# Optimization experiments

Hardware: AMD Instinct MI355X
Metric: run time of the kernel (lower is better)

## Reference

```python
import jax, jax.numpy as jnp
import numpy as np

L, B, H, E, V = 64, 2048, 1024, 50, 256  # seq_len, batch, hidden, char_emb, char_vocab
PAD = 0


def setup_inputs() -> dict:
    key = jax.random.key(0)
    ks = jax.random.split(key, 10)
    s = 1.0 / np.sqrt(H)  # torch LSTM default init scale
    emb = jax.random.normal(ks[0], (V, E), jnp.float32)
    emb = emb.at[PAD].set(0.0)  # padding_idx row
    return {
        "input": jax.random.randint(ks[1], (L, B), 0, V, jnp.int32),
        "h0": jax.random.normal(ks[2], (1, B, H), jnp.float32),
        "c0": jax.random.normal(ks[3], (1, B, H), jnp.float32),
        "emb": emb,
        "W_ih": jax.random.uniform(ks[4], (4 * H, E), jnp.float32, -s, s),
        "W_hh": jax.random.uniform(ks[5], (4 * H, H), jnp.float32, -s, s),
        "b_ih": jax.random.uniform(ks[6], (4 * H,), jnp.float32, -s, s),
        "b_hh": jax.random.uniform(ks[7], (4 * H,), jnp.float32, -s, s),
        "W_proj": jax.random.uniform(ks[8], (V, H), jnp.float32, -s, s),
        "b_proj": jax.random.uniform(ks[9], (V,), jnp.float32, -s, s),
    }


def reference(input, h0, c0, emb, W_ih, W_hh, b_ih, b_hh, W_proj, b_proj):
    # char embedding lookup: (L, B, E)
    x = emb[input]
    b = b_ih + b_hh

    def step(carry, x_t):
        h, c = carry  # (B, H) each
        gates = x_t @ W_ih.T + h @ W_hh.T + b  # (B, 4H), torch gate order i,f,g,o
        i, f, g, o = jnp.split(gates, 4, axis=-1)
        c_new = jax.nn.sigmoid(f) * c + jax.nn.sigmoid(i) * jnp.tanh(g)
        h_new = jax.nn.sigmoid(o) * jnp.tanh(c_new)
        return (h_new, c_new), h_new

    (hT, cT), hs = jax.lax.scan(step, (h0[0], c0[0]), x)
    # per-step linear projection of hidden state (same math as looped Linear)
    scores = hs @ W_proj.T + b_proj  # (L, B, V)
    return scores, hT[None], cT[None]
```

## Files before the change

kernel.cpp:

```cpp
#include <hip/hip_runtime.h>
#include <hip/hip_bf16.h>
#include <cstdint>
#include <cstddef>

#define LSEQ  64
#define BATCH 2048
#define HID   1024
#define NGATE 4096
#define VOC   256
#define EMBD  50

using bf16 = __hip_bfloat16;
typedef __attribute__((ext_vector_type(8))) __bf16 bf16x8;
typedef __attribute__((ext_vector_type(4))) float  f32x4;

__device__ __forceinline__ void gload_lds16(const void* g, void* l) {
  __builtin_amdgcn_global_load_lds(
      (const __attribute__((address_space(1))) unsigned int*)g,
      (__attribute__((address_space(3))) unsigned int*)l, 16, 0, 0);
}

__device__ __forceinline__ float sigf(float x) {
  x = fminf(fmaxf(x, -30.f), 30.f);
  return 1.f / (1.f + __expf(-x));
}
__device__ __forceinline__ float tanh_f(float x) {
  x = fminf(fmaxf(x, -15.f), 15.f);
  float e = __expf(2.f * x);
  return (e - 1.f) / (e + 1.f);
}

__device__ __forceinline__ void store_h_sys(bf16* p, float v) {
  union { __hip_bfloat16 b; unsigned short u; } cv;
  cv.b = __float2bfloat16(v);
  unsigned int d = cv.u;
  asm volatile("global_store_short %0, %1, off sc0 sc1" :: "v"(p), "v"(d) : "memory");
}


__global__ void k_prep_whh(const float* __restrict__ W, bf16* __restrict__ Wr) {
  size_t i = (size_t)blockIdx.x * 256 + threadIdx.x;
  int k  = (int)(i & 1023);
  int np = (int)(i >> 10);
  int T = np >> 7, w = np & 127;
  int wc = w >> 6, g = (w >> 4) & 3, hl = w & 15;
  int grow = g * HID + T * 32 + wc * 16 + hl;
  Wr[i] = __float2bfloat16(W[(size_t)grow * HID + k]);
}

__global__ void k_prep_embw(const float* __restrict__ emb, const float* __restrict__ W_ih,
                            const float* __restrict__ b_ih, const float* __restrict__ b_hh,
                            float* __restrict__ embW) {
  size_t i = (size_t)blockIdx.x * 256 + threadIdx.x;
  int np = (int)(i & 4095);
  int v  = (int)(i >> 12);
  int T = np >> 7, w = np & 127;
  int wc = w >> 6, g = (w >> 4) & 3, hl = w & 15;
  int grow = g * HID + T * 32 + wc * 16 + hl;
  float s = b_ih[grow] + b_hh[grow];
  #pragma unroll 10
  for (int e = 0; e < EMBD; ++e)
    s += emb[(size_t)v * EMBD + e] * W_ih[(size_t)grow * EMBD + e];
  embW[i] = s;
}

__global__ void k_prep_wp(const float* __restrict__ Wp_f, bf16* __restrict__ Wp) {
  size_t i = (size_t)blockIdx.x * 256 + threadIdx.x;
  Wp[i] = __float2bfloat16(Wp_f[i]);
}

__global__ void k_init_state(const float* __restrict__ h0, bf16* __restrict__ hs,
                             int* __restrict__ arr) {
  size_t i = (size_t)blockIdx.x * 256 + threadIdx.x;
  hs[i] = __float2bfloat16(h0[i]);
  if (i < 8320) arr[i] = 0;
}

__global__ __launch_bounds__(512) void g_persist(
    const float* __restrict__ c0, const bf16* __restrict__ Wr,
    bf16* __restrict__ hs, int* __restrict__ arr,
    const float* __restrict__ embW, const int* __restrict__ input,
    float* __restrict__ out, int nslots)
{
  __shared__ __align__(16) bf16 lsA[3 * 256 * 64];
  __shared__ __align__(16) bf16 lsB[3 * 128 * 64];

  const int tid  = threadIdx.x;
  const int wave = tid >> 6, lane = tid & 63;
  const int wr = wave >> 1, wc = wave & 1;
  const int hl = lane & 15, q = lane >> 4;

  const int u  = blockIdx.x >> 3;
  const int by = (blockIdx.x & 7) | ((u & 3) << 3);
  const int bx = u >> 2;
  const int bxbase = bx * 256;

  const bf16* Bsrc = Wr + (size_t)by * 128 * HID;

  size_t offA0, offA1, offA2, offA3;
  {
    int g0 = tid,      r0 = g0 >> 3, c0v = (g0 & 7) ^ (r0 & 7);
    int g1 = 512+tid,  r1 = g1 >> 3, c1v = (g1 & 7) ^ (r1 & 7);
    int g2 = 1024+tid, r2 = g2 >> 3, c2v = (g2 & 7) ^ (r2 & 7);
    int g3 = 1536+tid, r3 = g3 >> 3, c3v = (g3 & 7) ^ (r3 & 7);
    offA0 = (size_t)r0 * HID + c0v * 8;
    offA1 = (size_t)r1 * HID + c1v * 8;
    offA2 = (size_t)r2 * HID + c2v * 8;
    offA3 = (size_t)r3 * HID + c3v * 8;
  }
  bf16* dA = lsA + wave * 512;
  bf16* dB = lsB + wave * 512;

  int aofs0[4], aofs1[4], bofs0[4], bofs1[4];
  #pragma unroll
  for (int m = 0; m < 4; ++m) {
    int row = wr * 64 + m * 16 + hl;
    aofs0[m] = row * 64 + ((q ^ (hl & 7)) * 8);
    aofs1[m] = row * 64 + (((4 + q) ^ (hl & 7)) * 8);
  }
  #pragma unroll
  for (int n = 0; n < 4; ++n) {
    int row = wc * 64 + n * 16 + hl;
    bofs0[n] = row * 64 + ((q ^ (hl & 7)) * 8);
    bofs1[n] = row * 64 + (((4 + q) ^ (hl & 7)) * 8);
  }

  const int h_idx = by * 32 + wc * 16 + hl;
  float creg[4][4];
  #pragma unroll
  for (int m = 0; m < 4; ++m)
    #pragma unroll
    for (int r = 0; r < 4; ++r)
      creg[m][r] = c0[(size_t)(bxbase + wr * 64 + m * 16 + q * 4 + r) * HID + h_idx];

  const float* ewc = embW + (size_t)(by * 128 + wc * 64);
  const size_t slotE = (size_t)BATCH * HID;

#define SSTG0(S_) { gload_lds16(pA0, dA + (S_)*16384);         pA0 += 64;  \
                    gload_lds16(pA1, dA + (S_)*16384 + 4096);  pA1 += 64;  \
                    gload_lds16(pA2, dA + (S_)*16384 + 8192);  pA2 += 64; }
#define SSTG1(S_) { gload_lds16(pA3, dA + (S_)*16384 + 12288); pA3 += 64;  \
                    gload_lds16(pB0, dB + (S_)*8192);          pB0 += 64;  \
                    gload_lds16(pB1, dB + (S_)*8192 + 4096);   pB1 += 64; }

#define SPHASE(Ab_, Bb_, AO_, BO_, STG_) {                                  \
    bf16x8 aF[4], bF[4];                                                    \
    _Pragma("unroll")                                                       \
    for (int m = 0; m < 4; ++m) aF[m] = *(const bf16x8*)((Ab_) + AO_[m]);   \
    _Pragma("unroll")                                                       \
    for (int n = 0; n < 4; ++n) bF[n] = *(const bf16x8*)((Bb_) + BO_[n]);   \
    STG_;                                                                   \
    __builtin_amdgcn_s_barrier();                                           \
    asm volatile("s_waitcnt lgkmcnt(0)" ::: "memory");                      \
    __builtin_amdgcn_sched_barrier(0);                                      \
    __builtin_amdgcn_s_setprio(1);                                          \
    _Pragma("unroll")                                                       \
    for (int m = 0; m < 4; ++m)                                             \
      _Pragma("unroll")                                                     \
      for (int n = 0; n < 4; ++n)                                           \
        acc[m][n] = __builtin_amdgcn_mfma_f32_16x16x32_bf16(aF[m], bF[n], acc[m][n], 0, 0, 0); \
    __builtin_amdgcn_s_setprio(0);                                          \
  }

  for (int t = 0; t < LSEQ; ++t) {
    if (t) {
      if (tid == 0) {
        int it = 0;
        while (__hip_atomic_load(&arr[(t * 8 + bx) * 16], __ATOMIC_RELAXED,
                                 __HIP_MEMORY_SCOPE_AGENT) < 32 && ++it < (1 << 20))
          __builtin_amdgcn_s_sleep(2);
      }
      __syncthreads();
      __builtin_amdgcn_sched_barrier(0);
    }

    const bf16* Asrc = hs + (size_t)(t % nslots) * slotE + (size_t)bxbase * HID;
    const bf16 *pA0 = Asrc + offA0, *pA1 = Asrc + offA1;
    const bf16 *pA2 = Asrc + offA2, *pA3 = Asrc + offA3;
    const bf16 *pB0 = Bsrc + offA0, *pB1 = Bsrc + offA1;

    f32x4 acc[4][4] = {};

    SSTG0(0); SSTG1(0);
    SSTG0(1); SSTG1(1);
    __builtin_amdgcn_sched_barrier(0);

    int cur = 0, st = 2;
    for (int T = 0; T < 15; ++T) {
      asm volatile("s_waitcnt vmcnt(6)" ::: "memory");
      __builtin_amdgcn_s_barrier();
      const bf16* Ab = lsA + cur * 16384;
      const bf16* Bb = lsB + cur * 8192;
      if (T < 14) {
        SPHASE(Ab, Bb, aofs0, bofs0, SSTG0(st));
        SPHASE(Ab, Bb, aofs1, bofs1, SSTG1(st));
      } else {
        SPHASE(Ab, Bb, aofs0, bofs0, );
        SPHASE(Ab, Bb, aofs1, bofs1, );
      }
      cur = (cur == 2) ? 0 : cur + 1;
      st  = (st  == 2) ? 0 : st  + 1;
    }
    asm volatile("s_waitcnt vmcnt(0)" ::: "memory");
    __builtin_amdgcn_s_barrier();
    {
      const bf16* Ab = lsA + cur * 16384;
      const bf16* Bb = lsB + cur * 8192;
      SPHASE(Ab, Bb, aofs0, bofs0, );
      SPHASE(Ab, Bb, aofs1, bofs1, );
    }
    __builtin_amdgcn_sched_barrier(0);

    bf16* hout = hs + (size_t)((t + 1) % nslots) * slotE;
    #pragma unroll
    for (int m = 0; m < 4; ++m) {
      const int b0 = bxbase + wr * 64 + m * 16 + q * 4;
      const int4 iv = *(const int4*)(input + (size_t)t * BATCH + b0);
      #pragma unroll
      for (int r = 0; r < 4; ++r) {
        const int idx = (&iv.x)[r];
        const float* ew = ewc + (size_t)idx * NGATE;
        float gi = acc[m][0][r] + ew[hl];
        float gf = acc[m][1][r] + ew[16 + hl];
        float gg = acc[m][2][r] + ew[32 + hl];
        float go = acc[m][3][r] + ew[48 + hl];
        float cn = sigf(gf) * creg[m][r] + sigf(gi) * tanh_f(gg);
        float hn = sigf(go) * tanh_f(cn);
        creg[m][r] = cn;
        const size_t off = (size_t)(b0 + r) * HID + h_idx;
        store_h_sys(hout + off, hn);
        if (t == LSEQ - 1) {
          out[(size_t)LSEQ * BATCH * VOC + off] = hn;
          out[(size_t)LSEQ * BATCH * VOC + slotE + off] = cn;
        }
      }
    }

    __syncthreads();
    if (tid == 0)
      __hip_atomic_fetch_add(&arr[((t + 1) * 8 + bx) * 16], 1, __ATOMIC_RELAXED,
                             __HIP_MEMORY_SCOPE_AGENT);
  }
#undef SSTG0
#undef SSTG1
#undef SPHASE
}

template<int MODE>
__global__ __launch_bounds__(512) void g8(
    const bf16* __restrict__ Abase, const bf16* __restrict__ Bbase,
    const float* __restrict__ b_proj, float* __restrict__ out,
    int kc, int nslots)
{
  __shared__ __align__(16) bf16 lsA[3 * 256 * 64];
  __shared__ __align__(16) bf16 lsB[3 * 128 * 64];

  const int tid  = threadIdx.x;
  const int wave = tid >> 6, lane = tid & 63;
  const int wr = wave >> 1, wc = wave & 1;
  const int hl = lane & 15, q = lane >> 4;

  const int bx = blockIdx.x, by = blockIdx.y;

  int t_local = bx >> 3;
  int slot = (kc + 1 + t_local) % nslots;
  const bf16* Asrc = Abase + ((size_t)slot * BATCH + (size_t)(bx & 7) * 256) * HID;
  const bf16* Bsrc = Bbase + (size_t)by * 128 * HID;

  const bf16 *pA0, *pA1, *pA2, *pA3, *pB0, *pB1;
  {
    int g0 = tid,      r0 = g0 >> 3, c0v = (g0 & 7) ^ (r0 & 7);
    int g1 = 512+tid,  r1 = g1 >> 3, c1v = (g1 & 7) ^ (r1 & 7);
    int g2 = 1024+tid, r2 = g2 >> 3, c2v = (g2 & 7) ^ (r2 & 7);
    int g3 = 1536+tid, r3 = g3 >> 3, c3v = (g3 & 7) ^ (r3 & 7);
    pA0 = Asrc + (size_t)r0 * HID + c0v * 8;
    pA1 = Asrc + (size_t)r1 * HID + c1v * 8;
    pA2 = Asrc + (size_t)r2 * HID + c2v * 8;
    pA3 = Asrc + (size_t)r3 * HID + c3v * 8;
    pB0 = Bsrc + (size_t)r0 * HID + c0v * 8;
    pB1 = Bsrc + (size_t)r1 * HID + c1v * 8;
  }
  bf16* dA = lsA + wave * 512;
  bf16* dB = lsB + wave * 512;

  int aofs0[4], aofs1[4], bofs0[4], bofs1[4];
  #pragma unroll
  for (int m = 0; m < 4; ++m) {
    int row = wr * 64 + m * 16 + hl;
    aofs0[m] = row * 64 + ((q ^ (hl & 7)) * 8);
    aofs1[m] = row * 64 + (((4 + q) ^ (hl & 7)) * 8);
  }
  #pragma unroll
  for (int n = 0; n < 4; ++n) {
    int row = wc * 64 + n * 16 + hl;
    bofs0[n] = row * 64 + ((q ^ (hl & 7)) * 8);
    bofs1[n] = row * 64 + (((4 + q) ^ (hl & 7)) * 8);
  }

  f32x4 acc[4][4] = {};

#define STG_P0(S_) { gload_lds16(pA0, dA + (S_)*16384);         pA0 += 64;  \
                     gload_lds16(pA1, dA + (S_)*16384 + 4096);  pA1 += 64;  \
                     gload_lds16(pA2, dA + (S_)*16384 + 8192);  pA2 += 64; }
#define STG_P1(S_) { gload_lds16(pA3, dA + (S_)*16384 + 12288); pA3 += 64;  \
                     gload_lds16(pB0, dB + (S_)*8192);          pB0 += 64;  \
                     gload_lds16(pB1, dB + (S_)*8192 + 4096);   pB1 += 64; }

#define PHASE(Ab_, Bb_, AO_, BO_, STG_) {                                   \
    bf16x8 aF[4], bF[4];                                                    \
    _Pragma("unroll")                                                       \
    for (int m = 0; m < 4; ++m) aF[m] = *(const bf16x8*)((Ab_) + AO_[m]);   \
    _Pragma("unroll")                                                       \
    for (int n = 0; n < 4; ++n) bF[n] = *(const bf16x8*)((Bb_) + BO_[n]);   \
    STG_;                                                                   \
    __builtin_amdgcn_s_barrier();                                           \
    asm volatile("s_waitcnt lgkmcnt(0)" ::: "memory");                      \
    __builtin_amdgcn_sched_barrier(0);                                      \
    __builtin_amdgcn_s_setprio(1);                                          \
    _Pragma("unroll")                                                       \
    for (int m = 0; m < 4; ++m)                                             \
      _Pragma("unroll")                                                     \
      for (int n = 0; n < 4; ++n)                                           \
        acc[m][n] = __builtin_amdgcn_mfma_f32_16x16x32_bf16(aF[m], bF[n], acc[m][n], 0, 0, 0); \
    __builtin_amdgcn_s_setprio(0);                                          \
  }

  STG_P0(0); STG_P1(0);
  STG_P0(1); STG_P1(1);
  __builtin_amdgcn_sched_barrier(0);

  int cur = 0, st = 2;
  for (int T = 0; T < 15; ++T) {
    asm volatile("s_waitcnt vmcnt(6)" ::: "memory");
    __builtin_amdgcn_s_barrier();
    const bf16* Ab = lsA + cur * 16384;
    const bf16* Bb = lsB + cur * 8192;
    if (T < 14) {
      PHASE(Ab, Bb, aofs0, bofs0, STG_P0(st));
      PHASE(Ab, Bb, aofs1, bofs1, STG_P1(st));
    } else {
      PHASE(Ab, Bb, aofs0, bofs0, );
      PHASE(Ab, Bb, aofs1, bofs1, );
    }
    cur = (cur == 2) ? 0 : cur + 1;
    st  = (st  == 2) ? 0 : st  + 1;
  }
  asm volatile("s_waitcnt vmcnt(0)" ::: "memory");
  __builtin_amdgcn_s_barrier();
  {
    const bf16* Ab = lsA + cur * 16384;
    const bf16* Bb = lsB + cur * 8192;
    PHASE(Ab, Bb, aofs0, bofs0, );
    PHASE(Ab, Bb, aofs1, bofs1, );
  }

#undef STG_P0
#undef STG_P1
#undef PHASE

  const int qrow = q * 4;
  const int t_glob = kc + (bx >> 3);
  float* os = out + (size_t)t_glob * BATCH * VOC;
  const int b0base = (bx & 7) * 256 + wr * 64;
  #pragma unroll
  for (int m = 0; m < 4; ++m) {
    #pragma unroll
    for (int n = 0; n < 4; ++n) {
      const int v = by * 128 + wc * 64 + n * 16 + hl;
      const float bp = b_proj[v];
      #pragma unroll
      for (int r = 0; r < 4; ++r)
        os[(size_t)(b0base + m * 16 + qrow + r) * VOC + v] = acc[m][n][r] + bp;
    }
  }
}


extern "C" void kernel_launch(void* const* d_in, const int* in_sizes, int n_in,
                              void* d_out, int out_size, void* d_ws, size_t ws_size,
                              hipStream_t stream)
{
  (void)in_sizes; (void)n_in; (void)out_size; (void)ws_size;
  const int*   input  = (const int*)  d_in[0];
  const float* h0     = (const float*)d_in[1];
  const float* c0     = (const float*)d_in[2];
  const float* emb    = (const float*)d_in[3];
  const float* W_ih   = (const float*)d_in[4];
  const float* W_hh   = (const float*)d_in[5];
  const float* b_ih   = (const float*)d_in[6];
  const float* b_hh   = (const float*)d_in[7];
  const float* W_proj = (const float*)d_in[8];
  const float* b_proj = (const float*)d_in[9];
  float* out = (float*)d_out;

  char* ws = (char*)d_ws;
  bf16*  Wr   = (bf16*)(ws);
  bf16*  Wp   = (bf16*)(ws + 8388608);
  float* embW = (float*)(ws + 8912896);
  int*   arr  = (int*)  (ws + 13107200);
  bf16*  hs   = (bf16*) (ws + 13140480);
  const int nslots = 65;

  k_prep_whh <<<16384, 256, 0, stream>>>(W_hh, Wr);
  k_prep_wp  <<<1024,  256, 0, stream>>>(W_proj, Wp);
  k_prep_embw<<<4096,  256, 0, stream>>>(emb, W_ih, b_ih, b_hh, embW);
  k_init_state<<<8192, 256, 0, stream>>>(h0, hs, arr);

  g_persist<<<dim3(256), 512, 0, stream>>>(c0, Wr, hs, arr, embW, input, out, nslots);

  g8<1><<<dim3(8 * 64, 2), 512, 0, stream>>>(hs, Wp, b_proj, out, 0, nslots);
}
```

Measured before the change: 2.166 ms.

## Split persistent LSTM tiles to 128x128 with 4-stage K=32 pipeline

The persistent recurrent kernel moves from 256 blocks of 512 threads with 256x128 output tiles to 512 blocks of 256 threads with 128x128 tiles, two blocks per CU. The K loop now uses 32-wide tiles in a 4-deep LDS ring instead of 64-wide tiles in a 3-deep ring. The embedding-gate table is relaid so each (token, hidden) entry holds the four gates as one float4 load. Per-step barriers are indexed over 16 batch groups, and a vmcnt wait is added before signalling so h stores land first. The aim is better latency hiding and overlap between blocks per CU, at the cost of reading the W_hh tile twice as often.

```diff
diff --git a/kernel.cpp b/kernel.cpp
--- a/kernel.cpp
+++ b/kernel.cpp
@@ -52,11 +52,10 @@
                             const float* __restrict__ b_ih, const float* __restrict__ b_hh,
                             float* __restrict__ embW) {
   size_t i = (size_t)blockIdx.x * 256 + threadIdx.x;
-  int np = (int)(i & 4095);
-  int v  = (int)(i >> 12);
-  int T = np >> 7, w = np & 127;
-  int wc = w >> 6, g = (w >> 4) & 3, hl = w & 15;
-  int grow = g * HID + T * 32 + wc * 16 + hl;
+  int v     = (int)(i >> 12);
+  int h_col = (int)((i >> 2) & 1023);
+  int g     = (int)(i & 3);
+  int grow = g * HID + h_col;
   float s = b_ih[grow] + b_hh[grow];
   #pragma unroll 10
   for (int e = 0; e < EMBD; ++e)
@@ -73,57 +72,41 @@
                              int* __restrict__ arr) {
   size_t i = (size_t)blockIdx.x * 256 + threadIdx.x;
   hs[i] = __float2bfloat16(h0[i]);
-  if (i < 8320) arr[i] = 0;
-}
-
-__global__ __launch_bounds__(512) void g_persist(
+  if (i < 16640) arr[i] = 0;
+}
+
+__global__ __launch_bounds__(256, 2) void g_persist(
     const float* __restrict__ c0, const bf16* __restrict__ Wr,
     bf16* __restrict__ hs, int* __restrict__ arr,
     const float* __restrict__ embW, const int* __restrict__ input,
     float* __restrict__ out, int nslots)
 {
-  __shared__ __align__(16) bf16 lsA[3 * 256 * 64];
-  __shared__ __align__(16) bf16 lsB[3 * 128 * 64];
+  __shared__ __align__(16) bf16 lsA[4 * 128 * 32];
+  __shared__ __align__(16) bf16 lsB[4 * 128 * 32];
 
   const int tid  = threadIdx.x;
   const int wave = tid >> 6, lane = tid & 63;
   const int wr = wave >> 1, wc = wave & 1;
   const int hl = lane & 15, q = lane >> 4;
 
-  const int u  = blockIdx.x >> 3;
-  const int by = (blockIdx.x & 7) | ((u & 3) << 3);
+  const int u  = (int)blockIdx.x >> 3;
+  const int by = ((int)blockIdx.x & 7) | ((u & 3) << 3);
   const int bx = u >> 2;
-  const int bxbase = bx * 256;
+  const int bxbase = bx * 128;
 
   const bf16* Bsrc = Wr + (size_t)by * 128 * HID;
 
-  size_t offA0, offA1, offA2, offA3;
-  {
-    int g0 = tid,      r0 = g0 >> 3, c0v = (g0 & 7) ^ (r0 & 7);
-    int g1 = 512+tid,  r1 = g1 >> 3, c1v = (g1 & 7) ^ (r1 & 7);
-    int g2 = 1024+tid, r2 = g2 >> 3, c2v = (g2 & 7) ^ (r2 & 7);
-    int g3 = 1536+tid, r3 = g3 >> 3, c3v = (g3 & 7) ^ (r3 & 7);
-    offA0 = (size_t)r0 * HID + c0v * 8;
-    offA1 = (size_t)r1 * HID + c1v * 8;
-    offA2 = (size_t)r2 * HID + c2v * 8;
-    offA3 = (size_t)r3 * HID + c3v * 8;
-  }
+  const size_t off0 = (size_t)(tid >> 2) * HID +
+                      ((((tid & 3) ^ ((tid >> 4) & 3)) << 3));
   bf16* dA = lsA + wave * 512;
   bf16* dB = lsB + wave * 512;
 
-  int aofs0[4], aofs1[4], bofs0[4], bofs1[4];
-  #pragma unroll
-  for (int m = 0; m < 4; ++m) {
-    int row = wr * 64 + m * 16 + hl;
-    aofs0[m] = row * 64 + ((q ^ (hl & 7)) * 8);
-    aofs1[m] = row * 64 + (((4 + q) ^ (hl & 7)) * 8);
-  }
-  #pragma unroll
-  for (int n = 0; n < 4; ++n) {
-    int row = wc * 64 + n * 16 + hl;
-    bofs0[n] = row * 64 + ((q ^ (hl & 7)) * 8);
-    bofs1[n] = row * 64 + (((4 + q) ^ (hl & 7)) * 8);
-  }
+  const int kk = ((q ^ ((hl >> 2) & 3)) << 3);
+  int aofs[4], bofs[4];
+  #pragma unroll
+  for (int m = 0; m < 4; ++m) aofs[m] = (wr * 64 + m * 16 + hl) * 32 + kk;
+  #pragma unroll
+  for (int n = 0; n < 4; ++n) bofs[n] = (wc * 64 + n * 16 + hl) * 32 + kk;
 
   const int h_idx = by * 32 + wc * 16 + hl;
   float creg[4][4];
@@ -133,24 +116,21 @@
     for (int r = 0; r < 4; ++r)
       creg[m][r] = c0[(size_t)(bxbase + wr * 64 + m * 16 + q * 4 + r) * HID + h_idx];
 
-  const float* ewc = embW + (size_t)(by * 128 + wc * 64);
   const size_t slotE = (size_t)BATCH * HID;
 
-#define SSTG0(S_) { gload_lds16(pA0, dA + (S_)*16384);         pA0 += 64;  \
-                    gload_lds16(pA1, dA + (S_)*16384 + 4096);  pA1 += 64;  \
-                    gload_lds16(pA2, dA + (S_)*16384 + 8192);  pA2 += 64; }
-#define SSTG1(S_) { gload_lds16(pA3, dA + (S_)*16384 + 12288); pA3 += 64;  \
-                    gload_lds16(pB0, dB + (S_)*8192);          pB0 += 64;  \
-                    gload_lds16(pB1, dB + (S_)*8192 + 4096);   pB1 += 64; }
-
-#define SPHASE(Ab_, Bb_, AO_, BO_, STG_) {                                  \
+#define KSTG(S_) { gload_lds16(pA0, dA + (S_)*4096);        pA0 += 32;  \
+                   gload_lds16(pA1, dA + (S_)*4096 + 2048); pA1 += 32;  \
+                   gload_lds16(pB0, dB + (S_)*4096);        pB0 += 32;  \
+                   gload_lds16(pB1, dB + (S_)*4096 + 2048); pB1 += 32; }
+
+#define KTILE(CUR_) {                                                       \
+    const bf16* Ab = lsA + (CUR_) * 4096;                                   \
+    const bf16* Bb = lsB + (CUR_) * 4096;                                   \
     bf16x8 aF[4], bF[4];                                                    \
     _Pragma("unroll")                                                       \
-    for (int m = 0; m < 4; ++m) aF[m] = *(const bf16x8*)((Ab_) + AO_[m]);   \
-    _Pragma("unroll")                                                       \
-    for (int n = 0; n < 4; ++n) bF[n] = *(const bf16x8*)((Bb_) + BO_[n]);   \
-    STG_;                                                                   \
-    __builtin_amdgcn_s_barrier();                                           \
+    for (int m = 0; m < 4; ++m) aF[m] = *(const bf16x8*)(Ab + aofs[m]);     \
+    _Pragma("unroll")                                                       \
+    for (int n = 0; n < 4; ++n) bF[n] = *(const bf16x8*)(Bb + bofs[n]);     \
     asm volatile("s_waitcnt lgkmcnt(0)" ::: "memory");                      \
     __builtin_amdgcn_sched_barrier(0);                                      \
     __builtin_amdgcn_s_setprio(1);                                          \
@@ -166,7 +146,7 @@
     if (t) {
       if (tid == 0) {
         int it = 0;
-        while (__hip_atomic_load(&arr[(t * 8 + bx) * 16], __ATOMIC_RELAXED,
+        while (__hip_atomic_load(&arr[(t * 16 + bx) * 16], __ATOMIC_RELAXED,
                                  __HIP_MEMORY_SCOPE_AGENT) < 32 && ++it < (1 << 20))
           __builtin_amdgcn_s_sleep(2);
       }
@@ -175,40 +155,41 @@
     }
 
     const bf16* Asrc = hs + (size_t)(t % nslots) * slotE + (size_t)bxbase * HID;
-    const bf16 *pA0 = Asrc + offA0, *pA1 = Asrc + offA1;
-    const bf16 *pA2 = Asrc + offA2, *pA3 = Asrc + offA3;
-    const bf16 *pB0 = Bsrc + offA0, *pB1 = Bsrc + offA1;
+    const bf16 *pA0 = Asrc + off0, *pA1 = Asrc + 64 * HID + off0;
+    const bf16 *pB0 = Bsrc + off0, *pB1 = Bsrc + 64 * HID + off0;
 
     f32x4 acc[4][4] = {};
 
-    SSTG0(0); SSTG1(0);
-    SSTG0(1); SSTG1(1);
+    KSTG(0); KSTG(1);
     __builtin_amdgcn_sched_barrier(0);
 
-    int cur = 0, st = 2;
-    for (int T = 0; T < 15; ++T) {
-      asm volatile("s_waitcnt vmcnt(6)" ::: "memory");
+    for (int T = 0; T < 31; ++T) {
+      asm volatile("s_waitcnt vmcnt(4)" ::: "memory");
       __builtin_amdgcn_s_barrier();
-      const bf16* Ab = lsA + cur * 16384;
-      const bf16* Bb = lsB + cur * 8192;
-      if (T < 14) {
-        SPHASE(Ab, Bb, aofs0, bofs0, SSTG0(st));
-        SPHASE(Ab, Bb, aofs1, bofs1, SSTG1(st));
-      } else {
-        SPHASE(Ab, Bb, aofs0, bofs0, );
-        SPHASE(Ab, Bb, aofs1, bofs1, );
+      const int cur = T & 3;
+      {
+        const bf16* Ab = lsA + cur * 4096;
+        const bf16* Bb = lsB + cur * 4096;
+        bf16x8 aF[4], bF[4];
+        #pragma unroll
+        for (int m = 0; m < 4; ++m) aF[m] = *(const bf16x8*)(Ab + aofs[m]);
+        #pragma unroll
+        for (int n = 0; n < 4; ++n) bF[n] = *(const bf16x8*)(Bb + bofs[n]);
+        if (T < 30) KSTG((T + 2) & 3);
+        asm volatile("s_waitcnt lgkmcnt(0)" ::: "memory");
+        __builtin_amdgcn_sched_barrier(0);
+        __builtin_amdgcn_s_setprio(1);
+        #pragma unroll
+        for (int m = 0; m < 4; ++m)
+          #pragma unroll
+          for (int n = 0; n < 4; ++n)
+            acc[m][n] = __builtin_amdgcn_mfma_f32_16x16x32_bf16(aF[m], bF[n], acc[m][n], 0, 0, 0);
+        __builtin_amdgcn_s_setprio(0);
       }
-      cur = (cur == 2) ? 0 : cur + 1;
-      st  = (st  == 2) ? 0 : st  + 1;
     }
     asm volatile("s_waitcnt vmcnt(0)" ::: "memory");
     __builtin_amdgcn_s_barrier();
-    {
-      const bf16* Ab = lsA + cur * 16384;
-      const bf16* Bb = lsB + cur * 8192;
-      SPHASE(Ab, Bb, aofs0, bofs0, );
-      SPHASE(Ab, Bb, aofs1, bofs1, );
-    }
+    KTILE(3);
     __builtin_amdgcn_sched_barrier(0);
 
     bf16* hout = hs + (size_t)((t + 1) % nslots) * slotE;
@@ -219,11 +200,11 @@
       #pragma unroll
       for (int r = 0; r < 4; ++r) {
         const int idx = (&iv.x)[r];
-        const float* ew = ewc + (size_t)idx * NGATE;
-        float gi = acc[m][0][r] + ew[hl];
-        float gf = acc[m][1][r] + ew[16 + hl];
-        float gg = acc[m][2][r] + ew[32 + hl];
-        float go = acc[m][3][r] + ew[48 + hl];
+        const float4 e = *(const float4*)(embW + ((size_t)idx * 1024 + h_idx) * 4);
+        float gi = acc[m][0][r] + e.x;
+        float gf = acc[m][1][r] + e.y;
+        float gg = acc[m][2][r] + e.z;
+        float go = acc[m][3][r] + e.w;
         float cn = sigf(gf) * creg[m][r] + sigf(gi) * tanh_f(gg);
         float hn = sigf(go) * tanh_f(cn);
         creg[m][r] = cn;
@@ -236,14 +217,14 @@
       }
     }
 
+    asm volatile("s_waitcnt vmcnt(0)" ::: "memory");
     __syncthreads();
     if (tid == 0)
-      __hip_atomic_fetch_add(&arr[((t + 1) * 8 + bx) * 16], 1, __ATOMIC_RELAXED,
+      __hip_atomic_fetch_add(&arr[((t + 1) * 16 + bx) * 16], 1, __ATOMIC_RELAXED,
                              __HIP_MEMORY_SCOPE_AGENT);
   }
-#undef SSTG0
-#undef SSTG1
-#undef SPHASE
+#undef KSTG
+#undef KTILE
 }
 
 template<int MODE>
@@ -398,7 +379,7 @@
   bf16*  Wp   = (bf16*)(ws + 8388608);
   float* embW = (float*)(ws + 8912896);
   int*   arr  = (int*)  (ws + 13107200);
-  bf16*  hs   = (bf16*) (ws + 13140480);
+  bf16*  hs   = (bf16*) (ws + 13173760);
   const int nslots = 65;
 
   k_prep_whh <<<16384, 256, 0, stream>>>(W_hh, Wr);
@@ -406,7 +387,7 @@
   k_prep_embw<<<4096,  256, 0, stream>>>(emb, W_ih, b_ih, b_hh, embW);
   k_init_state<<<8192, 256, 0, stream>>>(h0, hs, arr);
 
-  g_persist<<<dim3(256), 512, 0, stream>>>(c0, Wr, hs, arr, embW, input, out, nslots);
+  g_persist<<<dim3(512), 256, 0, stream>>>(c0, Wr, hs, arr, embW, input, out, nslots);
 
   g8<1><<<dim3(8 * 64, 2), 512, 0, stream>>>(hs, Wp, b_proj, out, 0, nslots);
 }
```

New measurement: 2.499 ms. +15.4%, slower.
